# Performance work log

Measured on AMD Instinct MI355X. Metric: run time of the kernel, lower is better.

Reference implementation:

```python
import jax, jax.numpy as jnp
import numpy as np


def setup_inputs() -> dict:
    key = jax.random.key(0)
    k1, k2 = jax.random.split(key)
    x = jax.random.normal(k1, (16, 4096, 256), dtype=jnp.float32)
    embedding = jax.random.normal(k2, (1024, 256), dtype=jnp.float32)
    return {"x": x, "embedding": embedding}


def reference(x, embedding):
    # which_dim = -1 (default): no permute.
    shape = x.shape
    xf = x.reshape(-1, shape[-1])  # [N, D]
    x_sq = jnp.sum(xf * xf, axis=-1, keepdims=True)          # [N, 1]
    e_sq = jnp.sum(embedding * embedding, axis=-1)           # [K]
    dist = -(x_sq - 2.0 * (xf @ embedding.T) + e_sq[None, :])  # [N, K]
    embed_indices = jnp.argmax(dist, axis=1)                 # [N]
    embed_indices = embed_indices.reshape(shape[:-1])        # [B, S]
    quantization = embedding[embed_indices]                  # [B, S, D]
    return (quantization, embed_indices)
```

## Files before the change

kernel.cpp:

```cpp
#include <hip/hip_runtime.h>
#include <hip/hip_fp16.h>
#include <math.h>

#define MROWS   65536
#define NCODES  1024
#define KD      256
#define MARGIN  0.25f

typedef unsigned short u16;
typedef __attribute__((ext_vector_type(8))) _Float16 hfrag;
typedef __attribute__((ext_vector_type(4))) float f32x4;

#define IOFF ((size_t)MROWS * KD)

__device__ __forceinline__ float addrn(float a, float b) {
    float d; asm("v_add_f32 %0, %1, %2" : "=v"(d) : "v"(a), "v"(b)); return d;
}

__device__ __forceinline__ float sumsq_vf8ic4(const float* __restrict__ xr) {
    float a[4][8];
#pragma unroll
    for (int i = 0; i < 4; ++i)
#pragma unroll
        for (int l = 0; l < 8; ++l) a[i][l] = 0.f;
#pragma unroll
    for (int m = 0; m < 8; ++m)
#pragma unroll
        for (int i = 0; i < 4; ++i)
#pragma unroll
            for (int l = 0; l < 8; ++l) {
                float v = xr[m * 32 + i * 8 + l];
                a[i][l] = fmaf(v, v, a[i][l]);
            }
    float cc[8];
#pragma unroll
    for (int l = 0; l < 8; ++l)
        cc[l] = addrn(addrn(addrn(a[0][l], a[1][l]), a[2][l]), a[3][l]);
    float u0 = addrn(cc[0], cc[4]), u1 = addrn(cc[1], cc[5]);
    float u2 = addrn(cc[2], cc[6]), u3 = addrn(cc[3], cc[7]);
    return addrn(addrn(u0, u2), addrn(u1, u3));
}

__global__ __launch_bounds__(256)
void vq_pack(const float* __restrict__ src, u16* __restrict__ dh,
             unsigned int* __restrict__ cnt) {
    if (cnt && blockIdx.x == 0 && threadIdx.x == 0) *cnt = 0;
    __shared__ __align__(16) float lx[16 * 260];
    const int t = threadIdx.x;
    const size_t base = (size_t)blockIdx.x * 16 * 256;
#pragma unroll
    for (int qq = 0; qq < 4; ++qq) {
        int i4 = qq * 256 + t;
        int row = i4 >> 6, col = (i4 & 63) * 4;
        *(float4*)(lx + row * 260 + col) = *(const float4*)(src + base + (size_t)i4 * 4);
    }
    __syncthreads();
#pragma unroll
    for (int i = 0; i < 2; ++i) {
        int s = t + 256 * i;
        int kb = s >> 6, lane = s & 63;
        int r = lane & 15, kg = lane >> 4;
        int k0 = kb * 32 + kg * 8;
        u16 vh[8];
#pragma unroll
        for (int j = 0; j < 8; ++j) {
            float v = lx[r * 260 + k0 + j];
            vh[j] = __half_as_ushort(__float2half(v));
        }
        size_t off = (((size_t)blockIdx.x * 8 + kb) * 64 + lane) * 8;
        *(ulonglong2*)(dh + off) = *(ulonglong2*)vh;
    }
}

__global__ __launch_bounds__(256)
void vq_sumsq_llvm(const float* __restrict__ src, float* __restrict__ out) {
    __shared__ float lx[64 * 257];
    const int t = threadIdx.x;
    const size_t base = (size_t)blockIdx.x * 64 * 256;
#pragma unroll
    for (int qq = 0; qq < 16; ++qq) {
        int idx4 = qq * 256 + t;
        int row = idx4 >> 6, col4 = idx4 & 63;
        *(float4*)(lx + row * 257 + col4 * 4) = *(const float4*)(src + base + (size_t)idx4 * 4);
    }
    __syncthreads();
    if (t < 64) out[blockIdx.x * 64 + t] = sumsq_vf8ic4(lx + t * 257);
}

__global__ __launch_bounds__(256)
void vq_transpose(const float* __restrict__ emb, float* __restrict__ embT) {
    __shared__ float ld[64][65];
    const int t = threadIdx.x;
    const int c0 = blockIdx.x * 64, k0 = blockIdx.y * 64;
#pragma unroll
    for (int u = 0; u < 16; ++u) {
        int i = u * 256 + t;
        int r = i >> 6, col = i & 63;
        ld[r][col] = emb[(size_t)(c0 + r) * 256 + k0 + col];
    }
    __syncthreads();
#pragma unroll
    for (int u = 0; u < 16; ++u) {
        int i = u * 256 + t;
        int r = i >> 6, col = i & 63;
        embT[(size_t)(k0 + r) * 1024 + c0 + col] = ld[col][r];
    }
}

__global__ __launch_bounds__(256, 2)
void vq_gemm(const u16* __restrict__ Ah, const u16* __restrict__ Eh,
             const float* __restrict__ esq, float* __restrict__ tw) {
    extern __shared__ u16 lds[];
    u16* ldsA = lds;
    u16* ldsB = lds + 64 * 512;
    const int t = threadIdx.x;
    const int wave = t >> 6, lane = t & 63;
    const int wm = wave >> 1, wn = wave & 1;
    const int q = lane >> 4, c = lane & 15;
    const int m0 = blockIdx.x * 128;
    const int mrb8 = blockIdx.x * 64;

#pragma unroll
    for (int u = 0; u < 16; ++u) {
        int f = wave * 16 + u;
        const u16* srcp = Ah + ((size_t)(mrb8 + f) * 64 + lane) * 8;
        __builtin_amdgcn_global_load_lds((const unsigned int*)srcp,
                                         (unsigned int*)(ldsA + f * 512), 16, 0, 0);
    }
#pragma unroll
    for (int u = 0; u < 2; ++u) {
        int nf = wave * 2 + u;
        const u16* srcp = Eh + (((size_t)nf * 8 + 0) * 64 + lane) * 8;
        __builtin_amdgcn_global_load_lds((const unsigned int*)srcp,
                                         (unsigned int*)(ldsB + nf * 512), 16, 0, 0);
    }
    __syncthreads();

    float b1[16], s2v[16], bi[16];
#pragma unroll
    for (int r = 0; r < 16; ++r) { b1[r] = INFINITY; s2v[r] = INFINITY; bi[r] = 0.f; }

    f32x4 acc[4][4];
#pragma unroll
    for (int mi = 0; mi < 4; ++mi)
#pragma unroll
        for (int ni = 0; ni < 4; ++ni) acc[mi][ni] = 0.f;

    for (int step = 0; step < 64; ++step) {
        const int nqi = step >> 3, ks = step & 7, p = step & 1;
        if (step < 63) {
            const int ns = step + 1, nq2 = ns >> 3, ks2 = ns & 7, p2 = ns & 1;
#pragma unroll
            for (int u = 0; u < 2; ++u) {
                int nf = wave * 2 + u;
                const u16* srcp = Eh + (((size_t)(nq2 * 8 + nf) * 8 + ks2) * 64 + lane) * 8;
                __builtin_amdgcn_global_load_lds((const unsigned int*)srcp,
                                                 (unsigned int*)(ldsB + (p2 * 8 + nf) * 512), 16, 0, 0);
            }
        }
        hfrag af[4], bfv[4];
#pragma unroll
        for (int mi = 0; mi < 4; ++mi)
            af[mi] = *(const hfrag*)(ldsA + ((wm * 4 + mi) * 8 + ks) * 512 + lane * 8);
#pragma unroll
        for (int ni = 0; ni < 4; ++ni)
            bfv[ni] = *(const hfrag*)(ldsB + (p * 8 + wn * 4 + ni) * 512 + lane * 8);
#pragma unroll
        for (int mi = 0; mi < 4; ++mi)
#pragma unroll
            for (int ni = 0; ni < 4; ++ni)
                acc[mi][ni] = __builtin_amdgcn_mfma_f32_16x16x32_f16(af[mi], bfv[ni], acc[mi][ni], 0, 0, 0);

        if (ks == 7) {
#pragma unroll
            for (int ni = 0; ni < 4; ++ni) {
                const int code = nqi * 128 + wn * 64 + ni * 16 + c;
                const float e2 = esq[code];
                const float ci = (float)code;
#pragma unroll
                for (int mi = 0; mi < 4; ++mi)
#pragma unroll
                    for (int j = 0; j < 4; ++j) {
                        const int r = mi * 4 + j;
                        float sc = fmaf(-2.f, acc[mi][ni][j], e2);
                        bool lt = sc < b1[r];
                        s2v[r] = fminf(s2v[r], lt ? b1[r] : sc);
                        if (lt) { b1[r] = sc; bi[r] = ci; }
                    }
            }
#pragma unroll
            for (int mi = 0; mi < 4; ++mi)
#pragma unroll
                for (int ni = 0; ni < 4; ++ni) acc[mi][ni] = 0.f;
        }
        __syncthreads();
    }

#pragma unroll
    for (int r = 0; r < 16; ++r) {
#pragma unroll
        for (int mm = 1; mm < 16; mm <<= 1) {
            float ob = __shfl_xor(b1[r], mm, 64);
            float os = __shfl_xor(s2v[r], mm, 64);
            float oi = __shfl_xor(bi[r], mm, 64);
            if (ob < b1[r]) { s2v[r] = fminf(b1[r], os); b1[r] = ob; bi[r] = oi; }
            else            { s2v[r] = fminf(s2v[r], ob); }
        }
    }
    if (c == 0) {
#pragma unroll
        for (int mi = 0; mi < 4; ++mi)
#pragma unroll
            for (int j = 0; j < 4; ++j) {
                int row = m0 + wm * 64 + mi * 16 + q * 4 + j;
                size_t o = (size_t)row * 8 + wn * 4;
                int r = mi * 4 + j;
                tw[o + 0] = b1[r];
                tw[o + 1] = s2v[r];
                tw[o + 2] = bi[r];
            }
    }
}

__global__ void vq_reduce2(const float* __restrict__ tw, float* __restrict__ idxf,
                           unsigned int* __restrict__ cnt, int* __restrict__ list) {
    int row = blockIdx.x * 256 + threadIdx.x;
    float b0 = tw[(size_t)row * 8 + 0], s0 = tw[(size_t)row * 8 + 1], i0 = tw[(size_t)row * 8 + 2];
    float b1 = tw[(size_t)row * 8 + 4], s1 = tw[(size_t)row * 8 + 5], i1 = tw[(size_t)row * 8 + 6];
    float b, s2, bidx;
    if (b0 <= b1) { b = b0; bidx = i0; s2 = fminf(s0, b1); }
    else          { b = b1; bidx = i1; s2 = fminf(s1, b0); }
    idxf[row] = bidx;
    if (s2 - b < MARGIN) {
        unsigned int pos = atomicAdd(cnt, 1u);
        list[pos] = row;
    }
}

__global__ __launch_bounds__(256)
void vq_refine1(const float* __restrict__ x, const float* __restrict__ embT,
                const float* __restrict__ esq, const int* __restrict__ list,
                const unsigned int* __restrict__ cnt, float* __restrict__ idxf) {
    __shared__ __align__(16) float xs[8][260];
    __shared__ float xsq_s[8];
    __shared__ float lb[8][4];
    __shared__ int   li[8][4];
    const int t = threadIdx.x;
    const int wave = t >> 6, lane = t & 63;
    const unsigned int n = *cnt;
    float e2q[4];
#pragma unroll
    for (int qq = 0; qq < 4; ++qq) e2q[qq] = esq[qq * 256 + t];

    for (unsigned int g = blockIdx.x; g * 8u < n; g += gridDim.x) {
        const unsigned int r0 = g * 8u;
        const int nr = (int)min(8u, n - r0);
        __syncthreads();
#pragma unroll
        for (int u = 0; u < 2; ++u) {
            int s = u * 256 + t;
            int rr = s >> 6, l4 = s & 63;
            if (rr < nr) {
                int row = list[r0 + rr];
                *(float4*)(&xs[rr][l4 * 4]) = *(const float4*)(x + (size_t)row * 256 + l4 * 4);
            }
        }
        __syncthreads();
        if (t < nr) xsq_s[t] = sumsq_vf8ic4(&xs[t][0]);
        __syncthreads();

        float d[8][4];
#pragma unroll
        for (int r = 0; r < 8; ++r)
#pragma unroll
            for (int qq = 0; qq < 4; ++qq) d[r][qq] = 0.f;

        for (int kq = 0; kq < 64; ++kq) {
            float ev[4][4];
#pragma unroll
            for (int j = 0; j < 4; ++j)
#pragma unroll
                for (int qq = 0; qq < 4; ++qq)
                    ev[qq][j] = embT[(size_t)(kq * 4 + j) * 1024 + qq * 256 + t];
            float4 xf[8];
#pragma unroll
            for (int r = 0; r < 8; ++r) xf[r] = *(const float4*)(&xs[r][kq * 4]);
#pragma unroll
            for (int r = 0; r < 8; ++r)
#pragma unroll
                for (int qq = 0; qq < 4; ++qq) {
                    d[r][qq] = fmaf(xf[r].x, ev[qq][0], d[r][qq]);
                    d[r][qq] = fmaf(xf[r].y, ev[qq][1], d[r][qq]);
                    d[r][qq] = fmaf(xf[r].z, ev[qq][2], d[r][qq]);
                    d[r][qq] = fmaf(xf[r].w, ev[qq][3], d[r][qq]);
                }
        }
#pragma unroll
        for (int r = 0; r < 8; ++r) {
            float sv = INFINITY; int bc = 0x7fffffff;
#pragma unroll
            for (int qq = 0; qq < 4; ++qq) {
                float s = addrn(fmaf(-2.f, d[r][qq], xsq_s[r]), e2q[qq]);
                if (s < sv) { sv = s; bc = qq * 256 + t; }
            }
#pragma unroll
            for (int mm = 1; mm < 64; mm <<= 1) {
                float ob = __shfl_xor(sv, mm, 64);
                int oi = __shfl_xor(bc, mm, 64);
                if (ob < sv || (ob == sv && oi < bc)) { sv = ob; bc = oi; }
            }
            if (lane == 0) { lb[r][wave] = sv; li[r][wave] = bc; }
        }
        __syncthreads();
        if (t < nr) {
            float best = lb[t][0]; int bix = li[t][0];
#pragma unroll
            for (int w = 1; w < 4; ++w) {
                float ob = lb[t][w]; int oi = li[t][w];
                if (ob < best || (ob == best && oi < bix)) { best = ob; bix = oi; }
            }
            idxf[list[r0 + t]] = (float)bix;
        }
    }
}

__global__ void vq_gather(const float* __restrict__ emb, const float* __restrict__ idx_f,
                          float* __restrict__ qout) {
    int row = blockIdx.x * 4 + (threadIdx.x >> 6);
    int l = threadIdx.x & 63;
    int idx = (int)idx_f[row];
    float4 v = *(const float4*)(emb + (size_t)idx * KD + l * 4);
    *(float4*)(qout + (size_t)row * KD + l * 4) = v;
}

extern "C" void kernel_launch(void* const* d_in, const int* in_sizes, int n_in,
                              void* d_out, int out_size, void* d_ws, size_t ws_size,
                              hipStream_t stream) {
    const float* x   = (const float*)d_in[0];
    const float* emb = (const float*)d_in[1];
    float* out  = (float*)d_out;
    float* idxf = out + IOFF;

    u16* Ah = (u16*)out;
    float* embT = (float*)((char*)d_out + (32u << 20));

    char* ws = (char*)d_ws;
    u16* Eh    = (u16*)(ws);
    float* esq = (float*)(ws + (512 << 10));
    float* tw  = (float*)(ws + (1 << 20));
    unsigned int* cnt = (unsigned int*)(ws + ((size_t)3 << 20) + (512 << 10));
    int* list = (int*)(ws + ((size_t)3 << 20) + (512 << 10) + 256);

    vq_pack<<<dim3(MROWS / 16), dim3(256), 0, stream>>>(x, Ah, cnt);
    vq_pack<<<dim3(NCODES / 16), dim3(256), 0, stream>>>(emb, Eh, nullptr);
    vq_sumsq_llvm<<<dim3(NCODES / 64), dim3(256), 0, stream>>>(emb, esq);
    vq_transpose<<<dim3(16, 4), dim3(256), 0, stream>>>(emb, embT);
    vq_gemm<<<dim3(MROWS / 128), dim3(256), 81920, stream>>>(Ah, Eh, esq, tw);
    vq_reduce2<<<dim3(MROWS / 256), dim3(256), 0, stream>>>(tw, idxf, cnt, list);
    vq_refine1<<<dim3(512), dim3(256), 0, stream>>>(x, embT, esq, list, cnt, idxf);
    vq_gather<<<dim3(MROWS / 4), dim3(256), 0, stream>>>(emb, idxf, out);
}
```

Measured before the change: 140.6 us.

## Load B fragments directly from global into registers, drop per-step barrier

```diff
diff --git a/kernel.cpp b/kernel.cpp
--- a/kernel.cpp
+++ b/kernel.cpp
@@ -110,9 +110,7 @@
 __global__ __launch_bounds__(256, 2)
 void vq_gemm(const u16* __restrict__ Ah, const u16* __restrict__ Eh,
              const float* __restrict__ esq, float* __restrict__ tw) {
-    extern __shared__ u16 lds[];
-    u16* ldsA = lds;
-    u16* ldsB = lds + 64 * 512;
+    extern __shared__ u16 ldsA[];
     const int t = threadIdx.x;
     const int wave = t >> 6, lane = t & 63;
     const int wm = wave >> 1, wn = wave & 1;
@@ -127,15 +125,21 @@
         __builtin_amdgcn_global_load_lds((const unsigned int*)srcp,
                                          (unsigned int*)(ldsA + f * 512), 16, 0, 0);
     }
-#pragma unroll
-    for (int u = 0; u < 2; ++u) {
-        int nf = wave * 2 + u;
-        const u16* srcp = Eh + (((size_t)nf * 8 + 0) * 64 + lane) * 8;
-        __builtin_amdgcn_global_load_lds((const unsigned int*)srcp,
-                                         (unsigned int*)(ldsB + nf * 512), 16, 0, 0);
-    }
     __syncthreads();
 
+    auto LOADB = [&](int s, hfrag* dst) {
+        const int f0 = ((s >> 3) * 64) + (wn * 4) * 8 + (s & 7);
+#pragma unroll
+        for (int ni = 0; ni < 4; ++ni)
+            dst[ni] = *(const hfrag*)(Eh + (size_t)(f0 + ni * 8) * 512 + lane * 8);
+    };
+    auto LDA = [&](int s, hfrag* dst) {
+        const int ks = s & 7;
+#pragma unroll
+        for (int mi = 0; mi < 4; ++mi)
+            dst[mi] = *(const hfrag*)(ldsA + ((wm * 4 + mi) * 8 + ks) * 512 + lane * 8);
+    };
+
     float b1[16], s2v[16], bi[16];
 #pragma unroll
     for (int r = 0; r < 16; ++r) { b1[r] = INFINITY; s2v[r] = INFINITY; bi[r] = 0.f; }
@@ -146,32 +150,40 @@
 #pragma unroll
         for (int ni = 0; ni < 4; ++ni) acc[mi][ni] = 0.f;
 
-    for (int step = 0; step < 64; ++step) {
-        const int nqi = step >> 3, ks = step & 7, p = step & 1;
-        if (step < 63) {
-            const int ns = step + 1, nq2 = ns >> 3, ks2 = ns & 7, p2 = ns & 1;
-#pragma unroll
-            for (int u = 0; u < 2; ++u) {
-                int nf = wave * 2 + u;
-                const u16* srcp = Eh + (((size_t)(nq2 * 8 + nf) * 8 + ks2) * 64 + lane) * 8;
-                __builtin_amdgcn_global_load_lds((const unsigned int*)srcp,
-                                                 (unsigned int*)(ldsB + (p2 * 8 + nf) * 512), 16, 0, 0);
-            }
-        }
-        hfrag af[4], bfv[4];
-#pragma unroll
-        for (int mi = 0; mi < 4; ++mi)
-            af[mi] = *(const hfrag*)(ldsA + ((wm * 4 + mi) * 8 + ks) * 512 + lane * 8);
-#pragma unroll
-        for (int ni = 0; ni < 4; ++ni)
-            bfv[ni] = *(const hfrag*)(ldsB + (p * 8 + wn * 4 + ni) * 512 + lane * 8);
-#pragma unroll
-        for (int mi = 0; mi < 4; ++mi)
-#pragma unroll
-            for (int ni = 0; ni < 4; ++ni)
-                acc[mi][ni] = __builtin_amdgcn_mfma_f32_16x16x32_f16(af[mi], bfv[ni], acc[mi][ni], 0, 0, 0);
-
-        if (ks == 7) {
+    hfrag bA[4], bB[4];
+    LOADB(0, bA);
+    LOADB(1, bB);
+
+    for (int sp = 0; sp < 32; ++sp) {
+        const int s0 = sp * 2, s1 = sp * 2 + 1;
+        {
+            hfrag nx[4];
+            LOADB(s0 + 2 < 64 ? s0 + 2 : 0, nx);
+            hfrag af[4];
+            LDA(s0, af);
+#pragma unroll
+            for (int mi = 0; mi < 4; ++mi)
+#pragma unroll
+                for (int ni = 0; ni < 4; ++ni)
+                    acc[mi][ni] = __builtin_amdgcn_mfma_f32_16x16x32_f16(af[mi], bA[ni], acc[mi][ni], 0, 0, 0);
+#pragma unroll
+            for (int ni = 0; ni < 4; ++ni) bA[ni] = nx[ni];
+        }
+        {
+            hfrag nx[4];
+            LOADB(s1 + 2 < 64 ? s1 + 2 : 0, nx);
+            hfrag af[4];
+            LDA(s1, af);
+#pragma unroll
+            for (int mi = 0; mi < 4; ++mi)
+#pragma unroll
+                for (int ni = 0; ni < 4; ++ni)
+                    acc[mi][ni] = __builtin_amdgcn_mfma_f32_16x16x32_f16(af[mi], bB[ni], acc[mi][ni], 0, 0, 0);
+#pragma unroll
+            for (int ni = 0; ni < 4; ++ni) bB[ni] = nx[ni];
+        }
+        if ((s1 & 7) == 7) {
+            const int nqi = s1 >> 3;
 #pragma unroll
             for (int ni = 0; ni < 4; ++ni) {
                 const int code = nqi * 128 + wn * 64 + ni * 16 + c;
@@ -193,7 +205,6 @@
 #pragma unroll
                 for (int ni = 0; ni < 4; ++ni) acc[mi][ni] = 0.f;
         }
-        __syncthreads();
     }
 
 #pragma unroll
@@ -355,7 +366,7 @@
     vq_pack<<<dim3(NCODES / 16), dim3(256), 0, stream>>>(emb, Eh, nullptr);
     vq_sumsq_llvm<<<dim3(NCODES / 64), dim3(256), 0, stream>>>(emb, esq);
     vq_transpose<<<dim3(16, 4), dim3(256), 0, stream>>>(emb, embT);
-    vq_gemm<<<dim3(MROWS / 128), dim3(256), 81920, stream>>>(Ah, Eh, esq, tw);
+    vq_gemm<<<dim3(MROWS / 128), dim3(256), 65536, stream>>>(Ah, Eh, esq, tw);
     vq_reduce2<<<dim3(MROWS / 256), dim3(256), 0, stream>>>(tw, idxf, cnt, list);
     vq_refine1<<<dim3(512), dim3(256), 0, stream>>>(x, embT, esq, list, cnt, idxf);
     vq_gather<<<dim3(MROWS / 4), dim3(256), 0, stream>>>(emb, idxf, out);
```

Result: no change. 138.8 us (-1.2%).
